# Kernel tuning notes

Measured on AMD Instinct MI355X. Metric: run time of the kernel, lower is better.

The kernel has to match this reference:

```python
import jax, jax.numpy as jnp
import numpy as np

N = 50000
E = 400000
DIM_IN = 512
DIM_H = 64
HEADS = 8
DIM_OUT = 40
SLOPE = 0.2  # PyG GATv2Conv default negative_slope


def setup_inputs() -> dict:
    key = jax.random.key(0)
    ks = jax.random.split(key, 16)
    s = 0.05
    return {
        "x": jax.random.normal(ks[0], (N, DIM_IN), dtype=jnp.float32),
        "edge_index": jax.random.randint(ks[1], (2, E), 0, N, dtype=jnp.int64),
        "Wl1": jax.random.normal(ks[2], (DIM_IN, HEADS * DIM_H), dtype=jnp.float32) * s,
        "Wr1": jax.random.normal(ks[3], (DIM_IN, HEADS * DIM_H), dtype=jnp.float32) * s,
        "att1": jax.random.normal(ks[4], (HEADS, DIM_H), dtype=jnp.float32) * s,
        "b1": jax.random.normal(ks[5], (HEADS * DIM_H,), dtype=jnp.float32) * s,
        "Wl2": jax.random.normal(ks[6], (HEADS * DIM_H, DIM_OUT), dtype=jnp.float32) * s,
        "Wr2": jax.random.normal(ks[7], (HEADS * DIM_H, DIM_OUT), dtype=jnp.float32) * s,
        "att2": jax.random.normal(ks[8], (1, DIM_OUT), dtype=jnp.float32) * s,
        "b2": jax.random.normal(ks[9], (DIM_OUT,), dtype=jnp.float32) * s,
        "Wl3": jax.random.normal(ks[10], (HEADS * DIM_H, 2), dtype=jnp.float32) * s,
        "Wr3": jax.random.normal(ks[11], (HEADS * DIM_H, 2), dtype=jnp.float32) * s,
        "att3": jax.random.normal(ks[12], (1, 2), dtype=jnp.float32) * s,
        "b3": jax.random.normal(ks[13], (2,), dtype=jnp.float32) * s,
    }


def gatv2(x, src, dst, Wl, Wr, att, b):
    # PyG GATv2Conv: e_ij = att . LeakyReLU(W_l x_j + W_r x_i); softmax over j (by dst i);
    # out_i = sum_j alpha_ij * (W_l x_j); heads concatenated; bias added after.
    n = x.shape[0]
    H, F = att.shape
    xl = (x @ Wl).reshape(n, H, F)  # source transform
    xr = (x @ Wr).reshape(n, H, F)  # target transform
    e = jax.nn.leaky_relu(xl[src] + xr[dst], negative_slope=SLOPE)  # [E, H, F]
    logits = jnp.einsum("ehf,hf->eh", e, att)  # [E, H]
    m = jax.ops.segment_max(logits, dst, num_segments=n)  # self-loops => every segment nonempty
    ex = jnp.exp(logits - m[dst])
    denom = jax.ops.segment_sum(ex, dst, num_segments=n)
    alpha = ex / denom[dst]  # [E, H]
    out = jax.ops.segment_sum(xl[src] * alpha[:, :, None], dst, num_segments=n)  # [N, H, F]
    return out.reshape(n, H * F) + b


def reference(x, edge_index, Wl1, Wr1, att1, b1, Wl2, Wr2, att2, b2, Wl3, Wr3, att3, b3):
    # add self loops (PyG default add_self_loops=True)
    loops = jnp.arange(N, dtype=edge_index.dtype)
    ei = jnp.concatenate([edge_index, jnp.stack([loops, loops])], axis=1)
    src, dst = ei[0], ei[1]
    # eval mode: dropout is identity; ReverseLayerF is identity in forward
    h = jax.nn.relu(gatv2(x, src, dst, Wl1, Wr1, att1, b1))
    y_class = gatv2(h, src, dst, Wl2, Wr2, att2, b2)
    y_domain = gatv2(h, src, dst, Wl3, Wr3, att3, b3)
    return (y_class, y_domain)
```

## Files before the change

kernel.cpp:

```cpp
#include <hip/hip_runtime.h>
#include <math.h>

typedef unsigned short u16;
typedef unsigned int   u32;
typedef __attribute__((ext_vector_type(8))) short bf16x8;
typedef __attribute__((ext_vector_type(4))) float f32x4;
typedef __attribute__((ext_vector_type(4))) u32   u32x4;

__device__ __forceinline__ float b2f(u16 u) {
  union { u32 i; float f; } v; v.i = ((u32)u) << 16; return v.f;
}
__device__ __forceinline__ u16 f2b(float f) {
  union { u32 i; float f; } v; v.f = f;
  u32 r = v.i + 0x7FFFu + ((v.i >> 16) & 1u);
  return (u16)(r >> 16);
}
__device__ __forceinline__ float blo(u32 w) {
  union { u32 i; float f; } v; v.i = w << 16; return v.f;
}
__device__ __forceinline__ float bhi(u32 w) {
  union { u32 i; float f; } v; v.i = w & 0xFFFF0000u; return v.f;
}
__device__ __forceinline__ void ld_lds16(const u16* g, u16* l) {
  __builtin_amdgcn_global_load_lds((const __attribute__((address_space(1))) void*)g,
                                   (__attribute__((address_space(3))) void*)l, 16, 0, 0);
}

#define NN 50000
#define NE 400000
#define NT 450000
#define NBLK_SCAN 196

__global__ void k_detect(const void* x, const void* ei, int* flags) {
  __shared__ int cnt[2];
  int t = threadIdx.x;
  if (t < 2) cnt[t] = 0;
  __syncthreads();
  u16 u = ((const u16*)x)[t];
  int e = (u >> 7) & 0xFF;
  if (u == 0 || (e >= 90 && e <= 134)) atomicAdd(&cnt[0], 1);
  if (t < 16) {
    if (((const int*)ei)[2 * t + 1] == 0) atomicAdd(&cnt[1], 1);
  }
  __syncthreads();
  if (t == 0) {
    flags[0] = (cnt[0] >= 110) ? 1 : 0;
    flags[1] = (cnt[1] >= 15) ? 1 : 0;
  }
}

__device__ __forceinline__ int eidx(const int* ei, int pos, int i64) {
  return i64 ? ei[2 * pos] : ei[pos];
}

__global__ void k_convert_x(const void* x, const int* flags, u16* xb) {
  if (flags[0]) return;
  int c = blockIdx.x * 256 + threadIdx.x;
  const float* xf = (const float*)x + (size_t)c * 8;
  u32x4 o;
  #pragma unroll
  for (int i = 0; i < 4; ++i) {
    u32 lo = f2b(xf[2 * i]);
    u32 hi = f2b(xf[2 * i + 1]);
    o[i] = lo | (hi << 16);
  }
  *(u32x4*)(xb + (size_t)c * 8) = o;
}

__global__ void k_pack(const void* Wl1, const void* Wr1, const void* Wl2, const void* Wr2,
                       const void* Wl3, const void* Wr3, const void* att1, const void* b1,
                       const void* att2, const void* b2, const void* att3, const void* b3,
                       const int* flags, u16* w1t, u16* w23t, float* params) {
  int b = blockIdx.x;
  int isbf = flags[0];
  if (b < 2048) {
    int t = b * 256 + threadIdx.x;
    int r = t >> 9;
    int k = t & 511;
    const void* W = (r < 512) ? Wl1 : Wr1;
    int cc = r & 511;
    u16 v = isbf ? ((const u16*)W)[k * 512 + cc] : f2b(((const float*)W)[k * 512 + cc]);
    w1t[(size_t)r * 512 + k] = v;
  } else if (b < 2240) {
    int t = (b - 2048) * 256 + threadIdx.x;
    int k = t / 96;
    int c = t % 96;
    const void* W = nullptr; int idx = 0;
    if (c < 40)      { W = Wl2; idx = k * 40 + c; }
    else if (c < 42) { W = Wl3; idx = k * 2 + (c - 40); }
    else if (c < 82) { W = Wr2; idx = k * 40 + (c - 42); }
    else if (c < 84) { W = Wr3; idx = k * 2 + (c - 82); }
    u16 v = 0;
    if (W) v = isbf ? ((const u16*)W)[idx] : f2b(((const float*)W)[idx]);
    w23t[c * 512 + k] = v;
  } else {
    int t = (b - 2240) * 256 + threadIdx.x;
    if (t >= 1108) return;
    const void* src; int idx;
    if (t < 512)       { src = att1; idx = t; }
    else if (t < 1024) { src = b1;   idx = t - 512; }
    else if (t < 1064) { src = att2; idx = t - 1024; }
    else if (t < 1104) { src = b2;   idx = t - 1064; }
    else if (t < 1106) { src = att3; idx = t - 1104; }
    else               { src = b3;   idx = t - 1106; }
    params[t] = isbf ? b2f(((const u16*)src)[idx]) : ((const float*)src)[idx];
  }
}

__global__ void k_hist(const int* ei, const int* flags, int* deg) {
  int e = blockIdx.x * 256 + threadIdx.x;
  if (e >= NE) return;
  int d = eidx(ei, NE + e, flags[1]);
  atomicAdd(&deg[d], 1);
}

__global__ void k_scanA(const int* deg, int* row_ptr, int* bsum) {
  __shared__ int sh[256];
  int b = blockIdx.x, t = threadIdx.x;
  int i = b * 256 + t;
  int val = (i < NN) ? deg[i] + 1 : 0;
  sh[t] = val;
  __syncthreads();
  #pragma unroll
  for (int off = 1; off < 256; off <<= 1) {
    int v = (t >= off) ? sh[t - off] : 0;
    __syncthreads();
    sh[t] += v;
    __syncthreads();
  }
  if (i < NN) row_ptr[i] = sh[t] - val;
  if (t == 255) bsum[b] = sh[255];
}

__global__ void k_scanB(int* bsum, int* row_ptr) {
  __shared__ int sh[256];
  int t = threadIdx.x;
  int val = (t < NBLK_SCAN) ? bsum[t] : 0;
  sh[t] = val;
  __syncthreads();
  #pragma unroll
  for (int off = 1; off < 256; off <<= 1) {
    int v = (t >= off) ? sh[t - off] : 0;
    __syncthreads();
    sh[t] += v;
    __syncthreads();
  }
  if (t < NBLK_SCAN) bsum[t] = sh[t] - val;
  if (t == 255) row_ptr[NN] = sh[255];
}

__global__ void k_scanC(const int* bsum, int* row_ptr, int* cursor) {
  int i = blockIdx.x * 256 + threadIdx.x;
  if (i < NN) {
    int v = row_ptr[i] + bsum[blockIdx.x];
    row_ptr[i] = v;
    cursor[i] = v;
  }
}

__global__ void k_scatter(const int* ei, const int* flags, int* cursor, int* csr_src) {
  int t = blockIdx.x * 256 + threadIdx.x;
  if (t >= NT) return;
  int i64 = flags[1];
  int s, d;
  if (t < NE) { s = eidx(ei, t, i64); d = eidx(ei, NE + t, i64); }
  else        { s = d = t - NE; }
  int pos = atomicAdd(&cursor[d], 1);
  csr_src[pos] = s;
}

__global__ __launch_bounds__(256) void k_gemm1(const void* __restrict__ xraw, const u16* __restrict__ xb,
                                               const u16* __restrict__ Bt, const int* __restrict__ flags,
                                               u16* __restrict__ XL, u16* __restrict__ XR) {
  __shared__ __align__(16) u16 As[128 * 64];
  __shared__ __align__(16) u16 Bs[128 * 64];
  const int id  = blockIdx.x;
  const int xcd = id & 7;
  const int lb  = id >> 3;
  const int mt  = xcd * 49 + (lb >> 3);
  const int nt  = lb & 7;
  if (mt >= 391) return;
  const int m0 = mt * 128;
  const int n0 = nt * 128;
  const u16* __restrict__ A = flags[0] ? (const u16*)xraw : xb;
  const int t = threadIdx.x;
  const int wave = t >> 6;
  const int lane = t & 63;
  const int wm = (wave >> 1) * 64;
  const int wn = (wave & 1) * 64;
  const int fr = lane & 15;
  const int fk = lane >> 4;
  const int srow = lane >> 3;
  const int schk = (lane & 7) ^ srow;
  f32x4 acc[4][4] = {};
  for (int k0 = 0; k0 < 512; k0 += 64) {
    #pragma unroll
    for (int q = 0; q < 4; ++q) {
      int rbase = wave * 32 + q * 8;
      int gm = m0 + rbase + srow;
      if (gm > NN - 1) gm = NN - 1;
      ld_lds16(&A[(size_t)gm * 512 + k0 + schk * 8], &As[rbase * 64]);
      ld_lds16(&Bt[(size_t)(n0 + rbase + srow) * 512 + k0 + schk * 8], &Bs[rbase * 64]);
    }
    __syncthreads();
    #pragma unroll
    for (int h = 0; h < 2; ++h) {
      int s = h * 4 + fk;
      bf16x8 af[4], bb[4];
      #pragma unroll
      for (int i = 0; i < 4; ++i) {
        int row = wm + i * 16 + fr;
        af[i] = *(const bf16x8*)&As[row * 64 + ((s ^ (row & 7)) * 8)];
      }
      #pragma unroll
      for (int j = 0; j < 4; ++j) {
        int row = wn + j * 16 + fr;
        bb[j] = *(const bf16x8*)&Bs[row * 64 + ((s ^ (row & 7)) * 8)];
      }
      #pragma unroll
      for (int i = 0; i < 4; ++i)
        #pragma unroll
        for (int j = 0; j < 4; ++j)
          acc[i][j] = __builtin_amdgcn_mfma_f32_16x16x32_bf16(af[i], bb[j], acc[i][j], 0, 0, 0);
    }
    __syncthreads();
  }
  #pragma unroll
  for (int i = 0; i < 4; ++i) {
    #pragma unroll
    for (int r = 0; r < 4; ++r) {
      int gm = m0 + wm + i * 16 + fk * 4 + r;
      if (gm < NN) {
        #pragma unroll
        for (int j = 0; j < 4; ++j) {
          int gn = n0 + wn + j * 16 + fr;
          u16 v = f2b(acc[i][j][r]);
          if (gn < 512) XL[(size_t)gm * 512 + gn] = v;
          else          XR[(size_t)gm * 512 + gn - 512] = v;
        }
      }
    }
  }
}

__global__ __launch_bounds__(256) void k_gemm2(const u16* __restrict__ A, const u16* __restrict__ Bt,
                                               float* __restrict__ C) {
  __shared__ __align__(16) short As[128][40];
  __shared__ __align__(16) short Bs[96][40];
  const int m0 = blockIdx.x * 128;
  const int t = threadIdx.x;
  const int wave = t >> 6;
  const int lane = t & 63;
  const int fr = lane & 15;
  const int fk = lane >> 4;
  const int wm = wave * 32;
  f32x4 acc[2][6] = {};
  for (int k0 = 0; k0 < 512; k0 += 32) {
    #pragma unroll
    for (int h = 0; h < 2; ++h) {
      int c = t + h * 256;
      int row = c >> 2, kc = (c & 3) * 8;
      int gm = m0 + row;
      u32x4 va = {0, 0, 0, 0};
      if (gm < NN) va = *(const u32x4*)&A[(size_t)gm * 512 + k0 + kc];
      *(u32x4*)&As[row][kc] = va;
    }
    for (int c = t; c < 384; c += 256) {
      int row = c >> 2, kc = (c & 3) * 8;
      *(u32x4*)&Bs[row][kc] = *(const u32x4*)&Bt[row * 512 + k0 + kc];
    }
    __syncthreads();
    bf16x8 af[2], bb[6];
    #pragma unroll
    for (int i = 0; i < 2; ++i) af[i] = *(const bf16x8*)&As[wm + i * 16 + fr][fk * 8];
    #pragma unroll
    for (int j = 0; j < 6; ++j) bb[j] = *(const bf16x8*)&Bs[j * 16 + fr][fk * 8];
    #pragma unroll
    for (int i = 0; i < 2; ++i)
      #pragma unroll
      for (int j = 0; j < 6; ++j)
        acc[i][j] = __builtin_amdgcn_mfma_f32_16x16x32_bf16(af[i], bb[j], acc[i][j], 0, 0, 0);
    __syncthreads();
  }
  #pragma unroll
  for (int i = 0; i < 2; ++i) {
    #pragma unroll
    for (int j = 0; j < 6; ++j) {
      int gn = j * 16 + fr;
      if (gn < 84) {
        #pragma unroll
        for (int r = 0; r < 4; ++r) {
          int gm = m0 + wm + i * 16 + fk * 4 + r;
          if (gm < NN) C[(size_t)gm * 84 + gn] = acc[i][j][r];
        }
      }
    }
  }
}

__global__ __launch_bounds__(256) void k_layer1f(const u16* __restrict__ xl1, const u16* __restrict__ xr1,
                                                 const int* __restrict__ row_ptr, const int* __restrict__ csr_src,
                                                 const float* __restrict__ params, u16* __restrict__ hb) {
  int wid = blockIdx.x * 4 + (threadIdx.x >> 6);
  int lane = threadIdx.x & 63;
  int nw = gridDim.x * 4;
  float att4[8];
  #pragma unroll
  for (int k = 0; k < 8; ++k) att4[k] = 0.4f * params[lane * 8 + k];
  for (int i = wid; i < NN; i += nw) {
    int e0 = row_ptr[i], e1 = row_ptr[i + 1];
    u32x4 xrv = *(const u32x4*)&xr1[(size_t)i * 512 + lane * 8];
    float xr[8];
    #pragma unroll
    for (int q = 0; q < 4; ++q) { xr[2 * q] = blo(xrv[q]); xr[2 * q + 1] = bhi(xrv[q]); }
    float dp = 0.f;
    #pragma unroll
    for (int k = 0; k < 8; ++k) dp = fmaf(att4[k], 1.5f * xr[k], dp);
    dp += __shfl_xor(dp, 1, 64);
    dp += __shfl_xor(dp, 2, 64);
    dp += __shfl_xor(dp, 4, 64);
    float s = 0.f;
    float acc[8] = {0.f, 0.f, 0.f, 0.f, 0.f, 0.f, 0.f, 0.f};
    int q0 = csr_src[e0];
    int q1 = csr_src[e0 + 1 < e1 ? e0 + 1 : e1 - 1];
    int q2 = csr_src[e0 + 2 < e1 ? e0 + 2 : e1 - 1];
    int q3 = csr_src[e0 + 3 < e1 ? e0 + 3 : e1 - 1];
    for (int p = e0; p < e1; p += 4) {
      int j0 = q0, j1 = q1, j2 = q2, j3 = q3;
      u32x4 v0 = *(const u32x4*)&xl1[(size_t)j0 * 512 + lane * 8];
      u32x4 v1 = *(const u32x4*)&xl1[(size_t)j1 * 512 + lane * 8];
      u32x4 v2 = *(const u32x4*)&xl1[(size_t)j2 * 512 + lane * 8];
      u32x4 v3 = *(const u32x4*)&xl1[(size_t)j3 * 512 + lane * 8];
      int np = p + 4;
      if (np < e1) {
        q0 = csr_src[np];
        q1 = csr_src[np + 1 < e1 ? np + 1 : e1 - 1];
        q2 = csr_src[np + 2 < e1 ? np + 2 : e1 - 1];
        q3 = csr_src[np + 3 < e1 ? np + 3 : e1 - 1];
      }
      float m1 = (p + 1 < e1) ? 1.f : 0.f;
      float m2 = (p + 2 < e1) ? 1.f : 0.f;
      float m3 = (p + 3 < e1) ? 1.f : 0.f;
      float c0 = 0.f, c1 = 0.f, c2 = 0.f, c3 = 0.f;
      float xlv0[8], xlv1[8], xlv2[8], xlv3[8];
      #pragma unroll
      for (int q = 0; q < 4; ++q) {
        xlv0[2 * q] = blo(v0[q]); xlv0[2 * q + 1] = bhi(v0[q]);
        xlv1[2 * q] = blo(v1[q]); xlv1[2 * q + 1] = bhi(v1[q]);
        xlv2[2 * q] = blo(v2[q]); xlv2[2 * q + 1] = bhi(v2[q]);
        xlv3[2 * q] = blo(v3[q]); xlv3[2 * q + 1] = bhi(v3[q]);
      }
      #pragma unroll
      for (int k = 0; k < 8; ++k) {
        float t0 = xlv0[k] + xr[k];
        float t1 = xlv1[k] + xr[k];
        float t2 = xlv2[k] + xr[k];
        float t3 = xlv3[k] + xr[k];
        float u0 = fmaf(1.5f, xlv0[k], fabsf(t0));
        float u1 = fmaf(1.5f, xlv1[k], fabsf(t1));
        float u2 = fmaf(1.5f, xlv2[k], fabsf(t2));
        float u3 = fmaf(1.5f, xlv3[k], fabsf(t3));
        c0 = fmaf(att4[k], u0, c0);
        c1 = fmaf(att4[k], u1, c1);
        c2 = fmaf(att4[k], u2, c2);
        c3 = fmaf(att4[k], u3, c3);
      }
      c0 += __shfl_xor(c0, 1, 64); c1 += __shfl_xor(c1, 1, 64);
      c2 += __shfl_xor(c2, 1, 64); c3 += __shfl_xor(c3, 1, 64);
      c0 += __shfl_xor(c0, 2, 64); c1 += __shfl_xor(c1, 2, 64);
      c2 += __shfl_xor(c2, 2, 64); c3 += __shfl_xor(c3, 2, 64);
      c0 += __shfl_xor(c0, 4, 64); c1 += __shfl_xor(c1, 4, 64);
      c2 += __shfl_xor(c2, 4, 64); c3 += __shfl_xor(c3, 4, 64);
      float l0 = c0 + dp;
      float l1 = c1 + dp;
      float l2 = c2 + dp;
      float l3 = c3 + dp;
      float pv0 = __expf(fminf(fmaxf(l0, -30.f), 30.f));
      float pv1 = __expf(fminf(fmaxf(l1, -30.f), 30.f)) * m1;
      float pv2 = __expf(fminf(fmaxf(l2, -30.f), 30.f)) * m2;
      float pv3 = __expf(fminf(fmaxf(l3, -30.f), 30.f)) * m3;
      s += (pv0 + pv1) + (pv2 + pv3);
      #pragma unroll
      for (int k = 0; k < 8; ++k) {
        float a = fmaf(pv0, xlv0[k], acc[k]);
        a = fmaf(pv1, xlv1[k], a);
        a = fmaf(pv2, xlv2[k], a);
        acc[k] = fmaf(pv3, xlv3[k], a);
      }
    }
    float r = 1.f / s;
    u32x4 o;
    #pragma unroll
    for (int q = 0; q < 4; ++q) {
      u32 lo = f2b(fmaxf(fmaf(acc[2 * q],     r, params[512 + lane * 8 + 2 * q]),     0.f));
      u32 hi = f2b(fmaxf(fmaf(acc[2 * q + 1], r, params[512 + lane * 8 + 2 * q + 1]), 0.f));
      o[q] = lo | (hi << 16);
    }
    *(u32x4*)&hb[(size_t)i * 512 + lane * 8] = o;
  }
}

__global__ __launch_bounds__(256) void k_layer23f(const float* __restrict__ xlr23, const int* __restrict__ row_ptr,
                                                  const int* __restrict__ csr_src, const float* __restrict__ params,
                                                  const int* __restrict__ flags, void* __restrict__ out) {
  int wid = blockIdx.x * 4 + (threadIdx.x >> 6);
  int lane = threadIdx.x & 63;
  int nw = gridDim.x * 4;
  int e = lane >> 3;
  int g = lane & 7;
  int c0 = g * 5;
  float att2[5];
  #pragma unroll
  for (int u = 0; u < 5; ++u) att2[u] = params[1024 + c0 + u];
  float att3a = params[1104], att3b = params[1105];
  int isbf = flags[0];
  for (int i = wid; i < NN; i += nw) {
    int e0 = row_ptr[i], e1 = row_ptr[i + 1];
    const float* xri = &xlr23[(size_t)i * 84];
    float xr2[5];
    #pragma unroll
    for (int u = 0; u < 5; ++u) xr2[u] = xri[42 + c0 + u];
    float xr3a = xri[82], xr3b = xri[83];
    float s2 = 0.f, s3 = 0.f;
    float acc2[5] = {0.f, 0.f, 0.f, 0.f, 0.f};
    float acc3a = 0.f, acc3b = 0.f;
    int nit = (e1 - e0 + 7) >> 3;
    for (int it = 0; it < nit; ++it) {
      int p = e0 + it * 8 + e;
      bool valid = p < e1;
      int j = csr_src[valid ? p : e1 - 1];
      const float* xlj = &xlr23[(size_t)j * 84];
      float xl2[5];
      #pragma unroll
      for (int u = 0; u < 5; ++u) xl2[u] = xlj[c0 + u];
      float part = 0.f;
      #pragma unroll
      for (int u = 0; u < 5; ++u) {
        float t = xl2[u] + xr2[u];
        part = fmaf(att2[u], fmaxf(t, 0.2f * t), part);
      }
      part += __shfl_xor(part, 1, 64);
      part += __shfl_xor(part, 2, 64);
      part += __shfl_xor(part, 4, 64);
      float pv2 = valid ? __expf(fminf(fmaxf(part, -30.f), 30.f)) : 0.f;
      s2 += pv2;
      #pragma unroll
      for (int u = 0; u < 5; ++u) acc2[u] = fmaf(pv2, xl2[u], acc2[u]);
      if (g == 0) {
        float xl3a = xlj[40], xl3b = xlj[41];
        float ta = xl3a + xr3a, tb = xl3b + xr3b;
        float l3 = fmaf(att3a, fmaxf(ta, 0.2f * ta), att3b * fmaxf(tb, 0.2f * tb));
        float pv3 = valid ? __expf(fminf(fmaxf(l3, -30.f), 30.f)) : 0.f;
        s3 += pv3;
        acc3a = fmaf(pv3, xl3a, acc3a);
        acc3b = fmaf(pv3, xl3b, acc3b);
      }
    }
    #pragma unroll
    for (int m = 8; m <= 32; m <<= 1) {
      #pragma unroll
      for (int u = 0; u < 5; ++u) acc2[u] += __shfl_xor(acc2[u], m, 64);
      s2 += __shfl_xor(s2, m, 64);
      acc3a += __shfl_xor(acc3a, m, 64);
      acc3b += __shfl_xor(acc3b, m, 64);
      s3 += __shfl_xor(s3, m, 64);
    }
    if (e == 0) {
      float r2 = 1.f / s2;
      #pragma unroll
      for (int u = 0; u < 5; ++u) {
        float v = acc2[u] * r2 + params[1064 + c0 + u];
        size_t o = (size_t)i * 40 + c0 + u;
        if (isbf) ((u16*)out)[o] = f2b(v); else ((float*)out)[o] = v;
      }
      if (g == 0) {
        float r3 = 1.f / s3;
        float va = acc3a * r3 + params[1106];
        float vb = acc3b * r3 + params[1107];
        size_t o = 2000000 + (size_t)i * 2;
        if (isbf) { ((u16*)out)[o] = f2b(va); ((u16*)out)[o + 1] = f2b(vb); }
        else      { ((float*)out)[o] = va;    ((float*)out)[o + 1] = vb; }
      }
    }
  }
}

extern "C" void kernel_launch(void* const* d_in, const int* in_sizes, int n_in,
                              void* d_out, int out_size, void* d_ws, size_t ws_size,
                              hipStream_t stream) {
  const void* x    = d_in[0];
  const int*  ei   = (const int*)d_in[1];
  const void* Wl1  = d_in[2];
  const void* Wr1  = d_in[3];
  const void* att1 = d_in[4];
  const void* b1   = d_in[5];
  const void* Wl2  = d_in[6];
  const void* Wr2  = d_in[7];
  const void* att2 = d_in[8];
  const void* b2   = d_in[9];
  const void* Wl3  = d_in[10];
  const void* Wr3  = d_in[11];
  const void* att3 = d_in[12];
  const void* b3   = d_in[13];
  (void)in_sizes; (void)n_in; (void)out_size;

  char* ws = (char*)d_ws;
  size_t off = 0;
  auto alloc = [&](size_t bytes) -> void* {
    void* p = ws + off;
    off = (off + bytes + 255) & ~(size_t)255;
    return p;
  };
  int*   flags   = (int*)  alloc(64);
  u16*   xb      = (u16*)  alloc((size_t)NN * 512 * 2);
  u16*   w1t     = (u16*)  alloc((size_t)1024 * 512 * 2);
  u16*   xl1     = (u16*)  alloc((size_t)NN * 512 * 2);
  u16*   xr1     = (u16*)  alloc((size_t)NN * 512 * 2);
  u16*   hb      = (u16*)  alloc((size_t)NN * 512 * 2);
  u16*   w23t    = (u16*)  alloc((size_t)96 * 512 * 2);
  float* xlr23   = (float*)alloc((size_t)NN * 84 * 4);
  float* params  = (float*)alloc(1108 * 4);
  int*   row_ptr = (int*)  alloc((NN + 1) * 4);
  int*   deg     = (int*)  alloc(NN * 4);
  int*   cursor  = (int*)  alloc(NN * 4);
  int*   csr_src = (int*)  alloc((NT + 16) * 4);
  int*   bsum    = (int*)  alloc(256 * 4);
  if (ws_size < off) return;

  hipLaunchKernelGGL(k_detect, dim3(1), dim3(128), 0, stream, x, (const void*)ei, flags);
  hipLaunchKernelGGL(k_convert_x, dim3(12500), dim3(256), 0, stream, x, flags, xb);
  hipLaunchKernelGGL(k_pack, dim3(2245), dim3(256), 0, stream, Wl1, Wr1, Wl2, Wr2, Wl3, Wr3,
                     att1, b1, att2, b2, att3, b3, flags, w1t, w23t, params);
  hipMemsetAsync(deg, 0, NN * 4, stream);
  hipLaunchKernelGGL(k_hist, dim3((NE + 255) / 256), dim3(256), 0, stream, ei, flags, deg);
  hipLaunchKernelGGL(k_scanA, dim3(NBLK_SCAN), dim3(256), 0, stream, deg, row_ptr, bsum);
  hipLaunchKernelGGL(k_scanB, dim3(1), dim3(256), 0, stream, bsum, row_ptr);
  hipLaunchKernelGGL(k_scanC, dim3(NBLK_SCAN), dim3(256), 0, stream, bsum, row_ptr, cursor);
  hipLaunchKernelGGL(k_scatter, dim3((NT + 255) / 256), dim3(256), 0, stream, ei, flags, cursor, csr_src);
  hipLaunchKernelGGL(k_gemm1, dim3(3136), dim3(256), 0, stream, x, xb, w1t, flags, xl1, xr1);
  hipLaunchKernelGGL(k_layer1f, dim3(4096), dim3(256), 0, stream, xl1, xr1, row_ptr, csr_src, params, hb);
  hipLaunchKernelGGL(k_gemm2, dim3(391), dim3(256), 0, stream, hb, w23t, xlr23);
  hipLaunchKernelGGL(k_layer23f, dim3(4096), dim3(256), 0, stream, xlr23, row_ptr, csr_src, params, flags, d_out);
}
```

Before: 454.2 us.

## Double-buffer A tiles and load B fragments directly from global in GEMMs

Both GEMM kernels now double-buffer the A tile in shared memory, prefetching the next K-slice while the current one feeds the MFMAs, so each iteration needs only one barrier. The B operand is no longer staged through LDS; each wave reads its B fragments straight from global memory (L2-resident weights). This is meant to hide global-load latency and cut LDS traffic, at the cost of more global and L2 requests and extra registers, which could lower occupancy.

```diff
diff --git a/kernel.cpp b/kernel.cpp
--- a/kernel.cpp
+++ b/kernel.cpp
@@ -172,8 +172,7 @@
 __global__ __launch_bounds__(256) void k_gemm1(const void* __restrict__ xraw, const u16* __restrict__ xb,
                                                const u16* __restrict__ Bt, const int* __restrict__ flags,
                                                u16* __restrict__ XL, u16* __restrict__ XR) {
-  __shared__ __align__(16) u16 As[128 * 64];
-  __shared__ __align__(16) u16 Bs[128 * 64];
+  __shared__ __align__(16) u16 As[2][128 * 64];
   const int id  = blockIdx.x;
   const int xcd = id & 7;
   const int lb  = id >> 3;
@@ -192,38 +191,47 @@
   const int fk = lane >> 4;
   const int srow = lane >> 3;
   const int schk = (lane & 7) ^ srow;
-  f32x4 acc[4][4] = {};
-  for (int k0 = 0; k0 < 512; k0 += 64) {
+
+  auto stageA = [&](int buf, int k0) {
     #pragma unroll
     for (int q = 0; q < 4; ++q) {
       int rbase = wave * 32 + q * 8;
       int gm = m0 + rbase + srow;
       if (gm > NN - 1) gm = NN - 1;
-      ld_lds16(&A[(size_t)gm * 512 + k0 + schk * 8], &As[rbase * 64]);
-      ld_lds16(&Bt[(size_t)(n0 + rbase + srow) * 512 + k0 + schk * 8], &Bs[rbase * 64]);
-    }
-    __syncthreads();
+      ld_lds16(&A[(size_t)gm * 512 + k0 + schk * 8], &As[buf][rbase * 64]);
+    }
+  };
+
+  stageA(0, 0);
+  __syncthreads();
+  f32x4 acc[4][4] = {};
+  int cur = 0;
+  for (int ks = 0; ks < 8; ++ks) {
+    const int k0 = ks << 6;
+    bf16x8 breg[2][4];
+    #pragma unroll
+    for (int h = 0; h < 2; ++h)
+      #pragma unroll
+      for (int j = 0; j < 4; ++j)
+        breg[h][j] = *(const bf16x8*)&Bt[(size_t)(n0 + wn + j * 16 + fr) * 512 + k0 + (h * 4 + fk) * 8];
+    if (ks < 7) stageA(cur ^ 1, k0 + 64);
     #pragma unroll
     for (int h = 0; h < 2; ++h) {
       int s = h * 4 + fk;
-      bf16x8 af[4], bb[4];
+      bf16x8 af[4];
       #pragma unroll
       for (int i = 0; i < 4; ++i) {
         int row = wm + i * 16 + fr;
-        af[i] = *(const bf16x8*)&As[row * 64 + ((s ^ (row & 7)) * 8)];
-      }
-      #pragma unroll
-      for (int j = 0; j < 4; ++j) {
-        int row = wn + j * 16 + fr;
-        bb[j] = *(const bf16x8*)&Bs[row * 64 + ((s ^ (row & 7)) * 8)];
+        af[i] = *(const bf16x8*)&As[cur][row * 64 + ((s ^ (row & 7)) * 8)];
       }
       #pragma unroll
       for (int i = 0; i < 4; ++i)
         #pragma unroll
         for (int j = 0; j < 4; ++j)
-          acc[i][j] = __builtin_amdgcn_mfma_f32_16x16x32_bf16(af[i], bb[j], acc[i][j], 0, 0, 0);
+          acc[i][j] = __builtin_amdgcn_mfma_f32_16x16x32_bf16(af[i], breg[h][j], acc[i][j], 0, 0, 0);
     }
     __syncthreads();
+    cur ^= 1;
   }
   #pragma unroll
   for (int i = 0; i < 4; ++i) {
@@ -245,8 +253,7 @@
 
 __global__ __launch_bounds__(256) void k_gemm2(const u16* __restrict__ A, const u16* __restrict__ Bt,
                                                float* __restrict__ C) {
-  __shared__ __align__(16) short As[128][40];
-  __shared__ __align__(16) short Bs[96][40];
+  __shared__ __align__(16) short As[2][128][40];
   const int m0 = blockIdx.x * 128;
   const int t = threadIdx.x;
   const int wave = t >> 6;
@@ -255,32 +262,45 @@
   const int fk = lane >> 4;
   const int wm = wave * 32;
   f32x4 acc[2][6] = {};
-  for (int k0 = 0; k0 < 512; k0 += 32) {
-    #pragma unroll
-    for (int h = 0; h < 2; ++h) {
-      int c = t + h * 256;
-      int row = c >> 2, kc = (c & 3) * 8;
-      int gm = m0 + row;
-      u32x4 va = {0, 0, 0, 0};
-      if (gm < NN) va = *(const u32x4*)&A[(size_t)gm * 512 + k0 + kc];
-      *(u32x4*)&As[row][kc] = va;
-    }
-    for (int c = t; c < 384; c += 256) {
-      int row = c >> 2, kc = (c & 3) * 8;
-      *(u32x4*)&Bs[row][kc] = *(const u32x4*)&Bt[row * 512 + k0 + kc];
-    }
-    __syncthreads();
+  #pragma unroll
+  for (int h = 0; h < 2; ++h) {
+    int c = t + h * 256;
+    int row = c >> 2, kc = (c & 3) * 8;
+    int gm = m0 + row;
+    u32x4 va = {0, 0, 0, 0};
+    if (gm < NN) va = *(const u32x4*)&A[(size_t)gm * 512 + kc];
+    *(u32x4*)&As[0][row][kc] = va;
+  }
+  __syncthreads();
+  int cur = 0;
+  for (int ks = 0; ks < 16; ++ks) {
+    int k0 = ks * 32;
+    u32x4 nva0 = {0, 0, 0, 0}, nva1 = {0, 0, 0, 0};
+    if (ks < 15) {
+      int c0 = t, row0 = c0 >> 2, kc0 = (c0 & 3) * 8;
+      int c1 = t + 256, row1 = c1 >> 2, kc1 = (c1 & 3) * 8;
+      int gm0 = m0 + row0, gm1 = m0 + row1;
+      if (gm0 < NN) nva0 = *(const u32x4*)&A[(size_t)gm0 * 512 + k0 + 32 + kc0];
+      if (gm1 < NN) nva1 = *(const u32x4*)&A[(size_t)gm1 * 512 + k0 + 32 + kc1];
+    }
     bf16x8 af[2], bb[6];
     #pragma unroll
-    for (int i = 0; i < 2; ++i) af[i] = *(const bf16x8*)&As[wm + i * 16 + fr][fk * 8];
-    #pragma unroll
-    for (int j = 0; j < 6; ++j) bb[j] = *(const bf16x8*)&Bs[j * 16 + fr][fk * 8];
+    for (int j = 0; j < 6; ++j) bb[j] = *(const bf16x8*)&Bt[(size_t)(j * 16 + fr) * 512 + k0 + fk * 8];
+    #pragma unroll
+    for (int i = 0; i < 2; ++i) af[i] = *(const bf16x8*)&As[cur][wm + i * 16 + fr][fk * 8];
     #pragma unroll
     for (int i = 0; i < 2; ++i)
       #pragma unroll
       for (int j = 0; j < 6; ++j)
         acc[i][j] = __builtin_amdgcn_mfma_f32_16x16x32_bf16(af[i], bb[j], acc[i][j], 0, 0, 0);
+    if (ks < 15) {
+      int c0 = t, row0 = c0 >> 2, kc0 = (c0 & 3) * 8;
+      int c1 = t + 256, row1 = c1 >> 2, kc1 = (c1 & 3) * 8;
+      *(u32x4*)&As[cur ^ 1][row0][kc0] = nva0;
+      *(u32x4*)&As[cur ^ 1][row1][kc1] = nva1;
+    }
     __syncthreads();
+    cur ^= 1;
   }
   #pragma unroll
   for (int i = 0; i < 2; ++i) {
```

Result: slower. 502.0 us (+10.5%).
